# Performance work log

Hardware: AMD Instinct MI355X
Metric: run time of the kernel (lower is better)

## Reference

```python
import jax, jax.numpy as jnp
import numpy as np

N_USERS = 100000
N_ITEMS = 50001  # item_max + 1 (padding row 0)
N_EDGES = 1000000
D = 64
B = 4096
MAXLEN = 50
NUM_GNN_LAYERS = 2
LAMBDA_A = 0.5


def setup_inputs() -> dict:
    key = jax.random.key(0)
    ks = jax.random.split(key, 11)
    user_table = jax.random.normal(ks[0], (N_USERS, D), jnp.float32) * 0.1
    item_table = jax.random.normal(ks[1], (N_ITEMS, D), jnp.float32) * 0.1
    item_table = item_table.at[0].set(0.0)  # padding_idx=0
    edge_val_uv = jax.random.uniform(ks[2], (N_EDGES,), jnp.float32)
    edge_val_vu = jax.random.uniform(ks[3], (N_EDGES,), jnp.float32)
    W_att_w = jax.random.normal(ks[4], (D, D), jnp.float32) / jnp.sqrt(D)
    W_att_b = jax.random.normal(ks[5], (D,), jnp.float32) * 0.01
    W_agg = jax.random.normal(ks[6], (D, D), jnp.float32) / jnp.sqrt(D)
    edge_u = jax.random.randint(ks[7], (N_EDGES,), 0, N_USERS, jnp.int32)
    edge_i = jax.random.randint(ks[8], (N_EDGES,), 0, N_ITEMS, jnp.int32)
    user_idx = jax.random.randint(ks[9], (B,), 0, N_USERS, jnp.int32)
    ctx_items = jax.random.randint(ks[10], (B, MAXLEN), 0, N_ITEMS, jnp.int32)
    return dict(user_table=user_table, item_table=item_table,
                edge_val_uv=edge_val_uv, edge_val_vu=edge_val_vu,
                W_att_w=W_att_w, W_att_b=W_att_b, W_agg=W_agg,
                edge_u=edge_u, edge_i=edge_i, user_idx=user_idx,
                ctx_items=ctx_items)


def _propagate(V0, edge_u, edge_i, edge_val_uv, edge_val_vu):
    # V_{l+1} = VU @ (UV @ V_l), sparse bipartite spmm via segment sums
    V = V0
    layers = [V]
    for _ in range(NUM_GNN_LAYERS):
        u_msg = jax.ops.segment_sum(edge_val_uv[:, None] * V[edge_i],
                                    edge_u, num_segments=N_USERS)  # [U, D]
        V = jax.ops.segment_sum(edge_val_vu[:, None] * u_msg[edge_u],
                                edge_i, num_segments=N_ITEMS)       # [I, D]
        layers.append(V)
    return jnp.mean(jnp.stack(layers, 0), axis=0) + V0


def reference(user_table, item_table, edge_val_uv, edge_val_vu,
              W_att_w, W_att_b, W_agg,
              edge_u, edge_i, user_idx, ctx_items):
    # item_embedding_select: GNN propagation over bipartite graph
    V = _propagate(item_table, edge_u, edge_i, edge_val_uv, edge_val_vu)

    # forward_user
    id_emb = user_table[user_idx]          # [B, D]
    seq_emb = V[ctx_items]                  # [B, L, D]

    # user_attention_pooling
    key = jnp.tanh(jnp.einsum('bld,ed->ble', seq_emb, W_att_w) + W_att_b)
    attention = jnp.einsum('bld,bd->bl', key, id_emb)
    mask = jnp.sum(seq_emb, axis=-1) == 0   # [B, L]
    X = jnp.where(mask, 0.0, attention)
    eX = jnp.exp(X)
    attn = eX / (jnp.sum(eX, axis=1, keepdims=True) + 1e-12)
    pooled = jnp.einsum('bl,bld->bd', attn, seq_emb)
    out = pooled @ W_agg.T

    return LAMBDA_A * id_emb + (1.0 - LAMBDA_A) * out
```

## Files before the change

kernel.cpp:

```cpp
#include <hip/hip_runtime.h>

#define N_USERS 100000
#define N_ITEMS 50001
#define N_EDGES 1000000
#define D 64
#define BATCH 4096
#define MAXLEN 50

#define SHU 8
#define SHI 7
#define NBU ((N_USERS + 255) >> 8)
#define NBI ((N_ITEMS + 127) >> 7)
#define CAP 3072
#define BEPB 8192
#define BBLOCKS ((N_EDGES + BEPB - 1) / BEPB)

typedef __attribute__((ext_vector_type(8))) short short8;
typedef __attribute__((ext_vector_type(4))) float f32x4;

__device__ __forceinline__ float bf_lo(unsigned u) { return __uint_as_float(u << 16); }
__device__ __forceinline__ float bf_hi(unsigned u) { return __uint_as_float(u & 0xffff0000u); }
__device__ __forceinline__ float bf_s(unsigned short s) { return __uint_as_float(((unsigned)s) << 16); }
__device__ __forceinline__ unsigned bf_pack2(float a, float b) {
    unsigned ba = __float_as_uint(a);
    unsigned bb = __float_as_uint(b);
    ba += 0x7fffu + ((ba >> 16) & 1u);
    bb += 0x7fffu + ((bb >> 16) & 1u);
    return (ba >> 16) | (bb & 0xffff0000u);
}
__device__ __forceinline__ float fast_tanh(float x) {
    float e = __expf(2.0f * x);
    return 1.0f - 2.0f * __builtin_amdgcn_rcpf(e + 1.0f);
}

__global__ __launch_bounds__(256) void convert_kernel(
    const float* __restrict__ src, unsigned* __restrict__ dst, int npairs)
{
    int i = blockIdx.x * 256 + threadIdx.x;
    if (i < npairs) {
        float2 f = ((const float2*)src)[i];
        dst[i] = bf_pack2(f.x, f.y);
    }
}

__global__ __launch_bounds__(512) void bin_kernel(
    const int* __restrict__ eu, const int* __restrict__ ei,
    const float* __restrict__ ev_uv, const float* __restrict__ ev_vu,
    int* __restrict__ gcur_u, int* __restrict__ gcur_i,
    int2* __restrict__ staged_u, int2* __restrict__ staged_i)
{
    __shared__ int hist[NBU];
    __shared__ int runbase[NBU];
    __shared__ unsigned short rank[BEPB];
    int tid = threadIdx.x;
    int dir_i = (blockIdx.x >= BBLOCKS) ? 1 : 0;
    int blk = blockIdx.x - (dir_i ? BBLOCKS : 0);
    const int* erow = dir_i ? ei : eu;
    const int* esrc = dir_i ? eu : ei;
    const float* eval = dir_i ? ev_vu : ev_uv;
    int* gcur = dir_i ? gcur_i : gcur_u;
    int2* staged = dir_i ? staged_i : staged_u;
    const int shift = dir_i ? SHI : SHU;
    const float qs = dir_i ? 32767.0f : 65535.0f;
    const int rlmask = dir_i ? 127 : 255;
    const int nb = dir_i ? NBI : NBU;

    for (int i = tid; i < nb; i += 512) hist[i] = 0;
    __syncthreads();
    int e0 = blk * BEPB;
    for (int k = 0; k < BEPB / 512; ++k) {
        int slot = k * 512 + tid;
        int e = e0 + slot;
        if (e < N_EDGES)
            rank[slot] = (unsigned short)atomicAdd(&hist[erow[e] >> shift], 1);
    }
    __syncthreads();
    for (int i = tid; i < nb; i += 512) {
        int cn = hist[i];
        runbase[i] = cn ? (i * CAP + atomicAdd(&gcur[i], cn)) : 0;
    }
    __syncthreads();
    for (int k = 0; k < BEPB / 512; ++k) {
        int slot = k * 512 + tid;
        int e = e0 + slot;
        if (e < N_EDGES) {
            int row = erow[e];
            unsigned q = (unsigned)(fminf(fmaxf(eval[e], 0.0f), 1.0f) * qs + 0.5f);
            int2 en;
            en.x = (int)((unsigned)(row & rlmask) << 16 | q);
            en.y = esrc[e];
            staged[runbase[row >> shift] + rank[slot]] = en;
        }
    }
}

__global__ __launch_bounds__(256) void place_kernel(
    const int2* __restrict__ staged_u, const int2* __restrict__ staged_i,
    const int* __restrict__ gcur_u, const int* __restrict__ gcur_i,
    unsigned* __restrict__ csr_u, unsigned* __restrict__ csr_i,
    int2* __restrict__ offend_u, int2* __restrict__ offend_i)
{
    __shared__ int cnt[256];
    __shared__ int s[256];
    __shared__ int cur[256];
    int tid = threadIdx.x;
    int dir_i = (blockIdx.x >= NBU) ? 1 : 0;
    int b = blockIdx.x - (dir_i ? NBU : 0);
    const int2* staged = dir_i ? staged_i : staged_u;
    const int* gcur = dir_i ? gcur_i : gcur_u;
    unsigned* csr = dir_i ? csr_i : csr_u;
    int2* offend = dir_i ? offend_i : offend_u;
    const int NR = dir_i ? 128 : 256;
    const int nrows = dir_i ? N_ITEMS : N_USERS;
    const int idxbits = dir_i ? 17 : 16;

    int sb = b * CAP;
    int eb = sb + gcur[b];
    if (tid < NR) cnt[tid] = 0;
    __syncthreads();
    for (int idx = sb + tid; idx < eb; idx += 256) {
        int rl = ((unsigned)staged[idx].x) >> 16;
        atomicAdd(&cnt[rl], 1);
    }
    __syncthreads();
    int c = (tid < NR) ? cnt[tid] : 0;
    s[tid] = c;
    __syncthreads();
    for (int off = 1; off < 256; off <<= 1) {
        int v = (tid >= off) ? s[tid - off] : 0;
        __syncthreads();
        s[tid] += v;
        __syncthreads();
    }
    int excl = s[tid] - c;
    int row = b * NR + tid;
    if (tid < NR && row < nrows) {
        int2 oe; oe.x = sb + excl; oe.y = sb + excl + c;
        offend[row] = oe;
    }
    if (tid < NR) cur[tid] = sb + excl;
    __syncthreads();
    for (int idx = sb + tid; idx < eb; idx += 256) {
        int2 en = staged[idx];
        unsigned w0 = (unsigned)en.x;
        int rl = w0 >> 16;
        unsigned q = w0 & 0xFFFFu;
        int pos = atomicAdd(&cur[rl], 1);
        csr[pos] = (q << idxbits) | (unsigned)en.y;
    }
}

template<int IDXBITS>
__device__ __forceinline__ void gather_row_g8(
    const unsigned* __restrict__ src, const unsigned* __restrict__ csr,
    int o, int e, int c4, int g,
    float& A0, float& A1, float& A2, float& A3,
    float& A4, float& A5, float& A6, float& A7)
{
    constexpr unsigned MASK = (1u << IDXBITS) - 1u;
    constexpr float SCALE = 1.0f / (float)((1u << (32 - IDXBITS)) - 1u);
    float a0 = 0.f, a1 = 0.f, a2 = 0.f, a3 = 0.f;
    float a4 = 0.f, a5 = 0.f, a6 = 0.f, a7 = 0.f;
    for (int base = o; base < e; base += 8) {
        unsigned word = __builtin_nontemporal_load(csr + base + c4);
        uint4 u4[8];
        float v[8];
#pragma unroll
        for (int j = 0; j < 8; ++j) {
            unsigned wj = (unsigned)__shfl((int)word, 8 * g + j, 64);
            bool valid = (base + j) < e;
            int r = valid ? (int)(wj & MASK) : 0;
            v[j] = valid ? (float)(wj >> IDXBITS) * SCALE : 0.0f;
            u4[j] = *(const uint4*)(src + (size_t)r * 32 + 4 * c4);
        }
#pragma unroll
        for (int j = 0; j < 8; ++j) {
            a0 = fmaf(v[j], bf_lo(u4[j].x), a0);
            a1 = fmaf(v[j], bf_hi(u4[j].x), a1);
            a2 = fmaf(v[j], bf_lo(u4[j].y), a2);
            a3 = fmaf(v[j], bf_hi(u4[j].y), a3);
            a4 = fmaf(v[j], bf_lo(u4[j].z), a4);
            a5 = fmaf(v[j], bf_hi(u4[j].z), a5);
            a6 = fmaf(v[j], bf_lo(u4[j].w), a6);
            a7 = fmaf(v[j], bf_hi(u4[j].w), a7);
        }
    }
    A0 = a0; A1 = a1; A2 = a2; A3 = a3;
    A4 = a4; A5 = a5; A6 = a6; A7 = a7;
}

template<int IDXBITS>
__global__ __launch_bounds__(256) void gather_bf_kernel(
    const unsigned* __restrict__ src, const unsigned* __restrict__ csr,
    const int2* __restrict__ offend,
    unsigned* __restrict__ dst, int nrows)
{
    int gw = (blockIdx.x * 256 + threadIdx.x) >> 6;
    int lane = threadIdx.x & 63;
    int g = lane >> 3, c4 = lane & 7;
    int row = gw * 8 + g;
    int2 oe = (row < nrows) ? offend[row] : make_int2(0, 0);
    float a0, a1, a2, a3, a4, a5, a6, a7;
    gather_row_g8<IDXBITS>(src, csr, oe.x, oe.y, c4, g,
                           a0, a1, a2, a3, a4, a5, a6, a7);
    if (row < nrows) {
        uint4 o4;
        o4.x = bf_pack2(a0, a1);
        o4.y = bf_pack2(a2, a3);
        o4.z = bf_pack2(a4, a5);
        o4.w = bf_pack2(a6, a7);
        *((uint4*)(dst + (size_t)row * 32) + c4) = o4;
    }
}

__global__ __launch_bounds__(256) void gather_final_bf_kernel(
    const unsigned* __restrict__ src, const unsigned* __restrict__ csr,
    const int2* __restrict__ offend,
    const float* __restrict__ V0, const unsigned* __restrict__ V1bf,
    unsigned* __restrict__ Vf_bf)
{
    int gw = (blockIdx.x * 256 + threadIdx.x) >> 6;
    int lane = threadIdx.x & 63;
    int g = lane >> 3, c4 = lane & 7;
    int row = gw * 8 + g;
    int2 oe = (row < N_ITEMS) ? offend[row] : make_int2(0, 0);
    float a0, a1, a2, a3, a4, a5, a6, a7;
    gather_row_g8<17>(src, csr, oe.x, oe.y, c4, g,
                      a0, a1, a2, a3, a4, a5, a6, a7);
    if (row < N_ITEMS) {
        float4 v0a = *((const float4*)(V0 + (size_t)row * 64) + 2 * c4);
        float4 v0b = *((const float4*)(V0 + (size_t)row * 64) + 2 * c4 + 1);
        uint4 u1 = *((const uint4*)(V1bf + (size_t)row * 32) + c4);
        float r0 = (v0a.x + bf_lo(u1.x) + a0) * (1.0f / 3.0f) + v0a.x;
        float r1 = (v0a.y + bf_hi(u1.x) + a1) * (1.0f / 3.0f) + v0a.y;
        float r2 = (v0a.z + bf_lo(u1.y) + a2) * (1.0f / 3.0f) + v0a.z;
        float r3 = (v0a.w + bf_hi(u1.y) + a3) * (1.0f / 3.0f) + v0a.w;
        float r4 = (v0b.x + bf_lo(u1.z) + a4) * (1.0f / 3.0f) + v0b.x;
        float r5 = (v0b.y + bf_hi(u1.z) + a5) * (1.0f / 3.0f) + v0b.y;
        float r6 = (v0b.z + bf_lo(u1.w) + a6) * (1.0f / 3.0f) + v0b.z;
        float r7 = (v0b.w + bf_hi(u1.w) + a7) * (1.0f / 3.0f) + v0b.w;
        uint4 o4;
        o4.x = bf_pack2(r0, r1);
        o4.y = bf_pack2(r2, r3);
        o4.z = bf_pack2(r4, r5);
        o4.w = bf_pack2(r6, r7);
        *((uint4*)(Vf_bf + (size_t)row * 32) + c4) = o4;
    }
}

__global__ __launch_bounds__(256) void phase2_kernel(
    const float* __restrict__ user_table, const unsigned* __restrict__ Vf_bf,
    const float* __restrict__ Watt, const float* __restrict__ Wb,
    const float* __restrict__ Wagg, const int* __restrict__ uidx,
    const int* __restrict__ ctx, float* __restrict__ out)
{
    __shared__ __align__(16) unsigned seq[4][64 * 36];
    __shared__ unsigned short wgT[64 * 72];
    __shared__ __align__(16) float idrow[4][64];
    __shared__ float attn_l[4][64];
    __shared__ float pooled_l[4][64];

    const int tid = threadIdx.x;
    const int w = tid >> 6;
    const int lane = tid & 63;
    const int q = lane >> 4;
    const int n = lane & 15;
    const int b = blockIdx.x * 4 + w;

    for (int i = tid; i < 64 * 64; i += 256) {
        int e = i >> 6, d = i & 63;
        unsigned bb = __float_as_uint(Wagg[i]);
        bb += 0x7fffu + ((bb >> 16) & 1u);
        wgT[d * 72 + e] = (unsigned short)(bb >> 16);
    }
    __syncthreads();

    short8 wa_f[4][2];
#pragma unroll
    for (int et = 0; et < 4; ++et)
#pragma unroll
        for (int ks = 0; ks < 2; ++ks) {
            const float* rp = Watt + (size_t)(16 * et + n) * 64 + 32 * ks + 8 * q;
            float4 f0 = *(const float4*)rp;
            float4 f1 = *(const float4*)(rp + 4);
            union { short8 s; unsigned u[4]; } t;
            t.u[0] = bf_pack2(f0.x, f0.y);
            t.u[1] = bf_pack2(f0.z, f0.w);
            t.u[2] = bf_pack2(f1.x, f1.y);
            t.u[3] = bf_pack2(f1.z, f1.w);
            wa_f[et][ks] = t.s;
        }
    f32x4 biasv[4];
#pragma unroll
    for (int et = 0; et < 4; ++et)
        biasv[et] = *(const f32x4*)(Wb + 16 * et + 4 * q);
    short8 ones8;
#pragma unroll
    for (int j = 0; j < 8; ++j) ones8[j] = (short)0x3F80;

    int uid = uidx[b];
    idrow[w][lane] = user_table[(size_t)uid * 64 + lane];
    f32x4 idv[4];
#pragma unroll
    for (int et = 0; et < 4; ++et)
        idv[et] = *(f32x4*)&idrow[w][16 * et + 4 * q];

    int ci = (lane < MAXLEN) ? ctx[b * MAXLEN + lane] : 0;
#pragma unroll 5
    for (int it = 0; it < 25; ++it) {
        int l = 2 * it + (lane >> 5);
        int cc = lane & 31;
        int rsrc = __shfl(ci, l, 64);
        seq[w][l * 36 + cc] = Vf_bf[(size_t)rsrc * 32 + cc];
    }

    float xs[4];
#pragma unroll
    for (int lt = 0; lt < 4; ++lt) {
        union { short8 s; uint4 u; } B0, B1;
        B0.u = *(const uint4*)&seq[w][(16 * lt + n) * 36 + 4 * q];
        B1.u = *(const uint4*)&seq[w][(16 * lt + n) * 36 + 16 + 4 * q];

        f32x4 rsum = {0.f, 0.f, 0.f, 0.f};
        rsum = __builtin_amdgcn_mfma_f32_16x16x32_bf16(ones8, B0.s, rsum, 0, 0, 0);
        rsum = __builtin_amdgcn_mfma_f32_16x16x32_bf16(ones8, B1.s, rsum, 0, 0, 0);
        float rsv = rsum[0];

        float xacc = 0.0f;
#pragma unroll
        for (int et = 0; et < 4; ++et) {
            f32x4 a = {0.f, 0.f, 0.f, 0.f};
            a = __builtin_amdgcn_mfma_f32_16x16x32_bf16(wa_f[et][0], B0.s, a, 0, 0, 0);
            a = __builtin_amdgcn_mfma_f32_16x16x32_bf16(wa_f[et][1], B1.s, a, 0, 0, 0);
#pragma unroll
            for (int r = 0; r < 4; ++r) {
                float t = fast_tanh(a[r] + biasv[et][r]);
                xacc = fmaf(t, idv[et][r], xacc);
            }
        }
        xacc += __shfl_xor(xacc, 16, 64);
        xacc += __shfl_xor(xacc, 32, 64);
        xs[lt] = (rsv == 0.0f) ? 0.0f : xacc;
    }

    float ex[4];
    float tot = 0.0f;
#pragma unroll
    for (int lt = 0; lt < 4; ++lt) {
        int l = 16 * lt + n;
        ex[lt] = (l < MAXLEN) ? __expf(xs[lt]) : 0.0f;
        tot += ex[lt];
    }
    tot += __shfl_xor(tot, 1, 64);
    tot += __shfl_xor(tot, 2, 64);
    tot += __shfl_xor(tot, 4, 64);
    tot += __shfl_xor(tot, 8, 64);
    float inv = 1.0f / (tot + 1e-12f);
    if (lane < 16) {
#pragma unroll
        for (int lt = 0; lt < 4; ++lt)
            attn_l[w][16 * lt + lane] = ex[lt] * inv;
    }

    float pooled = 0.0f;
    for (int l = 0; l < MAXLEN; ++l) {
        float a = attn_l[w][l];
        unsigned uu = seq[w][l * 36 + (lane >> 1)];
        float sv = (lane & 1) ? bf_hi(uu) : bf_lo(uu);
        pooled = fmaf(a, sv, pooled);
    }
    pooled_l[w][lane] = pooled;

    float o = 0.0f;
#pragma unroll 8
    for (int d = 0; d < 64; ++d) {
        float pv = pooled_l[w][d];
        float wv = bf_s(wgT[d * 72 + lane]);
        o = fmaf(pv, wv, o);
    }
    out[(size_t)b * 64 + lane] = 0.5f * idrow[w][lane] + 0.5f * o;
}


extern "C" void kernel_launch(void* const* d_in, const int* in_sizes, int n_in,
                              void* d_out, int out_size, void* d_ws, size_t ws_size,
                              hipStream_t stream)
{
    const float* user_table = (const float*)d_in[0];
    const float* item_table = (const float*)d_in[1];
    const float* ev_uv      = (const float*)d_in[2];
    const float* ev_vu      = (const float*)d_in[3];
    const float* Watt       = (const float*)d_in[4];
    const float* Wb         = (const float*)d_in[5];
    const float* Wagg       = (const float*)d_in[6];
    const int*   edge_u     = (const int*)d_in[7];
    const int*   edge_i     = (const int*)d_in[8];
    const int*   uidx       = (const int*)d_in[9];
    const int*   ctx        = (const int*)d_in[10];
    float* out = (float*)d_out;

    const size_t NCAP = (size_t)NBU * CAP;

    char* p = (char*)d_ws;
    unsigned* it_bf    = (unsigned*)p; p += (size_t)N_ITEMS * 32 * 4;
    unsigned* u_msg_bf = (unsigned*)p; p += (size_t)N_USERS * 32 * 4;
    unsigned* V1_bf    = (unsigned*)p; p += (size_t)N_ITEMS * 32 * 4;
    char*     Sreg     = p;            p += NCAP * 8 * 2;
    int2*     staged_u = (int2*)Sreg;
    int2*     staged_i = (int2*)(Sreg + NCAP * 8);
    unsigned* Vf_bf    = (unsigned*)Sreg;
    unsigned* csr_u    = (unsigned*)p; p += NCAP * 4;
    unsigned* csr_i    = (unsigned*)p; p += NCAP * 4;
    int2*     offend_u = (int2*)p;     p += (size_t)N_USERS * 8;
    int2*     offend_i = (int2*)p;     p += (size_t)N_ITEMS * 8;
    int*      gcur_u   = (int*)p;      p += NBU * 4;
    int*      gcur_i   = (int*)p;      p += NBI * 4;

    hipMemsetAsync(gcur_u, 0, (NBU + NBI) * 4, stream);

    convert_kernel<<<(N_ITEMS * 32 + 255) / 256, 256, 0, stream>>>(
        item_table, it_bf, N_ITEMS * 32);

    bin_kernel<<<2 * BBLOCKS, 512, 0, stream>>>(edge_u, edge_i, ev_uv, ev_vu,
                                                gcur_u, gcur_i, staged_u, staged_i);
    place_kernel<<<NBU + NBI, 256, 0, stream>>>(staged_u, staged_i, gcur_u, gcur_i,
                                                csr_u, csr_i, offend_u, offend_i);

    const int ublocks = (N_USERS + 31) / 32;
    const int iblocks = (N_ITEMS + 31) / 32;

    gather_bf_kernel<16><<<ublocks, 256, 0, stream>>>(it_bf, csr_u, offend_u, u_msg_bf, N_USERS);
    gather_bf_kernel<17><<<iblocks, 256, 0, stream>>>(u_msg_bf, csr_i, offend_i, V1_bf, N_ITEMS);
    gather_bf_kernel<16><<<ublocks, 256, 0, stream>>>(V1_bf, csr_u, offend_u, u_msg_bf, N_USERS);
    gather_final_bf_kernel<<<iblocks, 256, 0, stream>>>(u_msg_bf, csr_i, offend_i,
                                                        item_table, V1_bf, Vf_bf);

    phase2_kernel<<<BATCH / 4, 256, 0, stream>>>(user_table, Vf_bf, Watt, Wb, Wagg,
                                                 uidx, ctx, out);
}
```

Measured before the change: 247.1 us.

## Replace binned CSR build with global count/scan/fill and prefetch seq rows

Replaces the two-stage bucketed binning (bin_kernel plus place_kernel, with a per-bucket staging area) with a direct CSR build: global atomic degree counts, a blockwise scan that claims row ranges through an atomic on a running total, and an atomic-cursor fill. This removes the staged intermediate buffer and its extra pass over the edges, but adds global atomic contention and scattered writes. In phase2, the context-row gather is issued as 16-byte loads before the weight setup so it overlaps with that work, and the shared-memory padding is tightened. Row segments are now placed in whatever order the blocks claim them, and edges within a row in atomic order, so the layout is no longer deterministic.

```diff
diff --git a/kernel.cpp b/kernel.cpp
--- a/kernel.cpp
+++ b/kernel.cpp
@@ -7,13 +7,9 @@
 #define BATCH 4096
 #define MAXLEN 50
 
-#define SHU 8
-#define SHI 7
-#define NBU ((N_USERS + 255) >> 8)
-#define NBI ((N_ITEMS + 127) >> 7)
-#define CAP 3072
-#define BEPB 8192
-#define BBLOCKS ((N_EDGES + BEPB - 1) / BEPB)
+#define NBU_S ((N_USERS + 255) / 256)
+#define NBI_S ((N_ITEMS + 255) / 256)
+#define EF_BLOCKS ((2 * N_EDGES + 255) / 256)
 
 typedef __attribute__((ext_vector_type(8))) short short8;
 typedef __attribute__((ext_vector_type(4))) float f32x4;
@@ -43,87 +39,32 @@
     }
 }
 
-__global__ __launch_bounds__(512) void bin_kernel(
+__global__ __launch_bounds__(256) void count_kernel(
     const int* __restrict__ eu, const int* __restrict__ ei,
-    const float* __restrict__ ev_uv, const float* __restrict__ ev_vu,
-    int* __restrict__ gcur_u, int* __restrict__ gcur_i,
-    int2* __restrict__ staged_u, int2* __restrict__ staged_i)
-{
-    __shared__ int hist[NBU];
-    __shared__ int runbase[NBU];
-    __shared__ unsigned short rank[BEPB];
+    int* __restrict__ cnt_u, int* __restrict__ cnt_i)
+{
+    int id = blockIdx.x * 256 + threadIdx.x;
+    if (id < N_EDGES) {
+        atomicAdd(&cnt_u[eu[id]], 1);
+    } else if (id < 2 * N_EDGES) {
+        atomicAdd(&cnt_i[ei[id - N_EDGES]], 1);
+    }
+}
+
+__global__ __launch_bounds__(256) void scan_kernel(
+    int* __restrict__ cnt_u, int* __restrict__ cnt_i, int* __restrict__ tot,
+    int2* __restrict__ offend_u, int2* __restrict__ offend_i)
+{
+    __shared__ int s[256];
+    __shared__ int base_s;
     int tid = threadIdx.x;
-    int dir_i = (blockIdx.x >= BBLOCKS) ? 1 : 0;
-    int blk = blockIdx.x - (dir_i ? BBLOCKS : 0);
-    const int* erow = dir_i ? ei : eu;
-    const int* esrc = dir_i ? eu : ei;
-    const float* eval = dir_i ? ev_vu : ev_uv;
-    int* gcur = dir_i ? gcur_i : gcur_u;
-    int2* staged = dir_i ? staged_i : staged_u;
-    const int shift = dir_i ? SHI : SHU;
-    const float qs = dir_i ? 32767.0f : 65535.0f;
-    const int rlmask = dir_i ? 127 : 255;
-    const int nb = dir_i ? NBI : NBU;
-
-    for (int i = tid; i < nb; i += 512) hist[i] = 0;
-    __syncthreads();
-    int e0 = blk * BEPB;
-    for (int k = 0; k < BEPB / 512; ++k) {
-        int slot = k * 512 + tid;
-        int e = e0 + slot;
-        if (e < N_EDGES)
-            rank[slot] = (unsigned short)atomicAdd(&hist[erow[e] >> shift], 1);
-    }
-    __syncthreads();
-    for (int i = tid; i < nb; i += 512) {
-        int cn = hist[i];
-        runbase[i] = cn ? (i * CAP + atomicAdd(&gcur[i], cn)) : 0;
-    }
-    __syncthreads();
-    for (int k = 0; k < BEPB / 512; ++k) {
-        int slot = k * 512 + tid;
-        int e = e0 + slot;
-        if (e < N_EDGES) {
-            int row = erow[e];
-            unsigned q = (unsigned)(fminf(fmaxf(eval[e], 0.0f), 1.0f) * qs + 0.5f);
-            int2 en;
-            en.x = (int)((unsigned)(row & rlmask) << 16 | q);
-            en.y = esrc[e];
-            staged[runbase[row >> shift] + rank[slot]] = en;
-        }
-    }
-}
-
-__global__ __launch_bounds__(256) void place_kernel(
-    const int2* __restrict__ staged_u, const int2* __restrict__ staged_i,
-    const int* __restrict__ gcur_u, const int* __restrict__ gcur_i,
-    unsigned* __restrict__ csr_u, unsigned* __restrict__ csr_i,
-    int2* __restrict__ offend_u, int2* __restrict__ offend_i)
-{
-    __shared__ int cnt[256];
-    __shared__ int s[256];
-    __shared__ int cur[256];
-    int tid = threadIdx.x;
-    int dir_i = (blockIdx.x >= NBU) ? 1 : 0;
-    int b = blockIdx.x - (dir_i ? NBU : 0);
-    const int2* staged = dir_i ? staged_i : staged_u;
-    const int* gcur = dir_i ? gcur_i : gcur_u;
-    unsigned* csr = dir_i ? csr_i : csr_u;
-    int2* offend = dir_i ? offend_i : offend_u;
-    const int NR = dir_i ? 128 : 256;
-    const int nrows = dir_i ? N_ITEMS : N_USERS;
-    const int idxbits = dir_i ? 17 : 16;
-
-    int sb = b * CAP;
-    int eb = sb + gcur[b];
-    if (tid < NR) cnt[tid] = 0;
-    __syncthreads();
-    for (int idx = sb + tid; idx < eb; idx += 256) {
-        int rl = ((unsigned)staged[idx].x) >> 16;
-        atomicAdd(&cnt[rl], 1);
-    }
-    __syncthreads();
-    int c = (tid < NR) ? cnt[tid] : 0;
+    int dir = (blockIdx.x >= NBU_S) ? 1 : 0;
+    int b = blockIdx.x - (dir ? NBU_S : 0);
+    int* cnt = dir ? cnt_i : cnt_u;
+    int2* offend = dir ? offend_i : offend_u;
+    const int nrows = dir ? N_ITEMS : N_USERS;
+    int row = b * 256 + tid;
+    int c = (row < nrows) ? cnt[row] : 0;
     s[tid] = c;
     __syncthreads();
     for (int off = 1; off < 256; off <<= 1) {
@@ -132,22 +73,36 @@
         s[tid] += v;
         __syncthreads();
     }
+    if (tid == 255) base_s = atomicAdd(&tot[dir], s[255]);
+    __syncthreads();
     int excl = s[tid] - c;
-    int row = b * NR + tid;
-    if (tid < NR && row < nrows) {
-        int2 oe; oe.x = sb + excl; oe.y = sb + excl + c;
-        offend[row] = oe;
-    }
-    if (tid < NR) cur[tid] = sb + excl;
-    __syncthreads();
-    for (int idx = sb + tid; idx < eb; idx += 256) {
-        int2 en = staged[idx];
-        unsigned w0 = (unsigned)en.x;
-        int rl = w0 >> 16;
-        unsigned q = w0 & 0xFFFFu;
-        int pos = atomicAdd(&cur[rl], 1);
-        csr[pos] = (q << idxbits) | (unsigned)en.y;
-    }
+    if (row < nrows) {
+        int start = base_s + excl;
+        offend[row] = make_int2(start, start + c);
+        cnt[row] = start;
+    }
+}
+
+__global__ __launch_bounds__(256) void fill_kernel(
+    const int* __restrict__ eu, const int* __restrict__ ei,
+    const float* __restrict__ ev_uv, const float* __restrict__ ev_vu,
+    int* __restrict__ cnt_u, int* __restrict__ cnt_i,
+    unsigned* __restrict__ csr_u, unsigned* __restrict__ csr_i)
+{
+    int id = blockIdx.x * 256 + threadIdx.x;
+    if (id >= 2 * N_EDGES) return;
+    int d = (id >= N_EDGES) ? 1 : 0;
+    int e = d ? id - N_EDGES : id;
+    int row = d ? ei[e] : eu[e];
+    int src = d ? eu[e] : ei[e];
+    float val = d ? ev_vu[e] : ev_uv[e];
+    const float qs = d ? 32767.0f : 65535.0f;
+    const int idxbits = d ? 17 : 16;
+    unsigned q = (unsigned)(fminf(fmaxf(val, 0.0f), 1.0f) * qs + 0.5f);
+    int* cnt = d ? cnt_i : cnt_u;
+    unsigned* csr = d ? csr_i : csr_u;
+    int pos = atomicAdd(&cnt[row], 1);
+    csr[pos] = (q << idxbits) | (unsigned)src;
 }
 
 template<int IDXBITS>
@@ -254,8 +209,8 @@
     const float* __restrict__ Wagg, const int* __restrict__ uidx,
     const int* __restrict__ ctx, float* __restrict__ out)
 {
-    __shared__ __align__(16) unsigned seq[4][64 * 36];
-    __shared__ unsigned short wgT[64 * 72];
+    __shared__ __align__(16) unsigned seq[4][50 * 36];
+    __shared__ unsigned short wgT[64 * 65];
     __shared__ __align__(16) float idrow[4][64];
     __shared__ float attn_l[4][64];
     __shared__ float pooled_l[4][64];
@@ -267,11 +222,21 @@
     const int n = lane & 15;
     const int b = blockIdx.x * 4 + w;
 
+    int ci = (lane < MAXLEN) ? ctx[b * MAXLEN + lane] : 0;
+    const int g8 = lane >> 3, c4v = lane & 7;
+    uint4 vv[7];
+#pragma unroll
+    for (int bt = 0; bt < 7; ++bt) {
+        int l = bt * 8 + g8;
+        int rsrc = __shfl(ci, l, 64);
+        vv[bt] = *((const uint4*)(Vf_bf + (size_t)rsrc * 32) + c4v);
+    }
+
     for (int i = tid; i < 64 * 64; i += 256) {
         int e = i >> 6, d = i & 63;
         unsigned bb = __float_as_uint(Wagg[i]);
         bb += 0x7fffu + ((bb >> 16) & 1u);
-        wgT[d * 72 + e] = (unsigned short)(bb >> 16);
+        wgT[d * 65 + e] = (unsigned short)(bb >> 16);
     }
     __syncthreads();
 
@@ -305,13 +270,11 @@
     for (int et = 0; et < 4; ++et)
         idv[et] = *(f32x4*)&idrow[w][16 * et + 4 * q];
 
-    int ci = (lane < MAXLEN) ? ctx[b * MAXLEN + lane] : 0;
-#pragma unroll 5
-    for (int it = 0; it < 25; ++it) {
-        int l = 2 * it + (lane >> 5);
-        int cc = lane & 31;
-        int rsrc = __shfl(ci, l, 64);
-        seq[w][l * 36 + cc] = Vf_bf[(size_t)rsrc * 32 + cc];
+#pragma unroll
+    for (int bt = 0; bt < 7; ++bt) {
+        int l = bt * 8 + g8;
+        if (l < MAXLEN)
+            *(uint4*)&seq[w][l * 36 + 4 * c4v] = vv[bt];
     }
 
     float xs[4];
@@ -375,7 +338,7 @@
 #pragma unroll 8
     for (int d = 0; d < 64; ++d) {
         float pv = pooled_l[w][d];
-        float wv = bf_s(wgT[d * 72 + lane]);
+        float wv = bf_s(wgT[d * 65 + lane]);
         o = fmaf(pv, wv, o);
     }
     out[(size_t)b * 64 + lane] = 0.5f * idrow[w][lane] + 0.5f * o;
@@ -399,32 +362,29 @@
     const int*   ctx        = (const int*)d_in[10];
     float* out = (float*)d_out;
 
-    const size_t NCAP = (size_t)NBU * CAP;
-
     char* p = (char*)d_ws;
     unsigned* it_bf    = (unsigned*)p; p += (size_t)N_ITEMS * 32 * 4;
     unsigned* u_msg_bf = (unsigned*)p; p += (size_t)N_USERS * 32 * 4;
     unsigned* V1_bf    = (unsigned*)p; p += (size_t)N_ITEMS * 32 * 4;
-    char*     Sreg     = p;            p += NCAP * 8 * 2;
-    int2*     staged_u = (int2*)Sreg;
-    int2*     staged_i = (int2*)(Sreg + NCAP * 8);
-    unsigned* Vf_bf    = (unsigned*)Sreg;
-    unsigned* csr_u    = (unsigned*)p; p += NCAP * 4;
-    unsigned* csr_i    = (unsigned*)p; p += NCAP * 4;
+    unsigned* Vf_bf    = (unsigned*)p; p += (size_t)N_ITEMS * 32 * 4;
+    unsigned* csr_u    = (unsigned*)p; p += (size_t)(N_EDGES + 16) * 4;
+    unsigned* csr_i    = (unsigned*)p; p += (size_t)(N_EDGES + 16) * 4;
     int2*     offend_u = (int2*)p;     p += (size_t)N_USERS * 8;
     int2*     offend_i = (int2*)p;     p += (size_t)N_ITEMS * 8;
-    int*      gcur_u   = (int*)p;      p += NBU * 4;
-    int*      gcur_i   = (int*)p;      p += NBI * 4;
-
-    hipMemsetAsync(gcur_u, 0, (NBU + NBI) * 4, stream);
+    int*      cnt_u    = (int*)p;      p += (size_t)N_USERS * 4;
+    int*      cnt_i    = (int*)p;      p += (size_t)N_ITEMS * 4;
+    int*      tot      = (int*)p;      p += 2 * 4;
+
+    hipMemsetAsync(cnt_u, 0, (size_t)(N_USERS + N_ITEMS + 2) * 4, stream);
 
     convert_kernel<<<(N_ITEMS * 32 + 255) / 256, 256, 0, stream>>>(
         item_table, it_bf, N_ITEMS * 32);
 
-    bin_kernel<<<2 * BBLOCKS, 512, 0, stream>>>(edge_u, edge_i, ev_uv, ev_vu,
-                                                gcur_u, gcur_i, staged_u, staged_i);
-    place_kernel<<<NBU + NBI, 256, 0, stream>>>(staged_u, staged_i, gcur_u, gcur_i,
-                                                csr_u, csr_i, offend_u, offend_i);
+    count_kernel<<<EF_BLOCKS, 256, 0, stream>>>(edge_u, edge_i, cnt_u, cnt_i);
+    scan_kernel<<<NBU_S + NBI_S, 256, 0, stream>>>(cnt_u, cnt_i, tot,
+                                                   offend_u, offend_i);
+    fill_kernel<<<EF_BLOCKS, 256, 0, stream>>>(edge_u, edge_i, ev_uv, ev_vu,
+                                               cnt_u, cnt_i, csr_u, csr_i);
 
     const int ublocks = (N_USERS + 31) / 32;
     const int iblocks = (N_ITEMS + 31) / 32;
```

Result: slower. 456.4 us (+84.6%).
